# Kernel tuning notes

Hardware: AMD Instinct MI355X
Metric: run time of the kernel (lower is better)

## Reference

```python
import jax, jax.numpy as jnp
import numpy as np

STATE_DIM = 512
HIDDEN = 256
ACTION = 8
BATCH = 32768
LN_EPS = 1e-5


def setup_inputs() -> dict:
    key = jax.random.key(0)
    ks = jax.random.split(key, 24)
    s = 0.02
    inp = {
        'initial_state': jax.random.normal(ks[0], (BATCH, STATE_DIM), jnp.float32),
        'final_state': jax.random.normal(ks[1], (BATCH, STATE_DIM), jnp.float32),
        'horizon': 10,
        # fc: Linear(1024->256), LayerNorm(256), ReLU, Linear(256->256), ReLU
        'W1': jax.random.normal(ks[2], (HIDDEN, 2 * STATE_DIM), jnp.float32) * s,
        'b1': jnp.zeros((HIDDEN,), jnp.float32),
        'ln_g': jnp.ones((HIDDEN,), jnp.float32),
        'ln_b': jnp.zeros((HIDDEN,), jnp.float32),
        'W2': jax.random.normal(ks[3], (HIDDEN, HIDDEN), jnp.float32) * s,
        'b2': jnp.zeros((HIDDEN,), jnp.float32),
        # GRU layer 0 (input=ACTION) and layer 1 (input=HIDDEN)
        'Wih0': jax.random.normal(ks[4], (3 * HIDDEN, ACTION), jnp.float32) * s,
        'Whh0': jax.random.normal(ks[5], (3 * HIDDEN, HIDDEN), jnp.float32) * s,
        'bih0': jnp.zeros((3 * HIDDEN,), jnp.float32),
        'bhh0': jnp.zeros((3 * HIDDEN,), jnp.float32),
        'Wih1': jax.random.normal(ks[6], (3 * HIDDEN, HIDDEN), jnp.float32) * s,
        'Whh1': jax.random.normal(ks[7], (3 * HIDDEN, HIDDEN), jnp.float32) * s,
        'bih1': jnp.zeros((3 * HIDDEN,), jnp.float32),
        'bhh1': jnp.zeros((3 * HIDDEN,), jnp.float32),
        # fc_action: 256 -> 8
        'Wa': jax.random.normal(ks[8], (ACTION, HIDDEN), jnp.float32) * s,
        'ba': jnp.zeros((ACTION,), jnp.float32),
        # fc_init_hidden: 256 -> 512
        'Winit': jax.random.normal(ks[9], (2 * HIDDEN, HIDDEN), jnp.float32) * s,
        'binit': jnp.zeros((2 * HIDDEN,), jnp.float32),
    }
    return inp


def _gru_cell(x, h, Wih, Whh, bih, bhh):
    # torch.nn.GRU cell: gates ordered [r, z, n]
    gi = x @ Wih.T + bih              # [B, 3H]
    gh = h @ Whh.T + bhh              # [B, 3H]
    i_r, i_z, i_n = jnp.split(gi, 3, axis=-1)
    h_r, h_z, h_n = jnp.split(gh, 3, axis=-1)
    r = jax.nn.sigmoid(i_r + h_r)
    z = jax.nn.sigmoid(i_z + h_z)
    n = jnp.tanh(i_n + r * h_n)
    return (1.0 - z) * n + z * h


def reference(initial_state, final_state, horizon, W1, b1, ln_g, ln_b, W2, b2,
              Wih0, Whh0, bih0, bhh0, Wih1, Whh1, bih1, bhh1, Wa, ba, Winit, binit):
    B = initial_state.shape[0]
    combined = jnp.concatenate([initial_state, final_state], axis=-1)  # [B, 2*state]
    h = combined @ W1.T + b1
    mu = jnp.mean(h, axis=-1, keepdims=True)
    var = jnp.var(h, axis=-1, keepdims=True)
    h = (h - mu) * jax.lax.rsqrt(var + LN_EPS) * ln_g + ln_b
    h = jax.nn.relu(h)
    h = jax.nn.relu(h @ W2.T + b2)    # [B, H]

    # Replicates torch .view(2, B, H) on a [B, 2H] tensor (row-major reshape)
    hidden = jnp.reshape(h @ Winit.T + binit, (2, B, HIDDEN))
    h0, h1 = hidden[0], hidden[1]
    a0 = jnp.zeros((B, ACTION), initial_state.dtype)

    def step(carry, _):
        h0, h1, a = carry
        h0n = _gru_cell(a, h0, Wih0, Whh0, bih0, bhh0)
        h1n = _gru_cell(h0n, h1, Wih1, Whh1, bih1, bhh1)
        logits = h1n @ Wa.T + ba       # [B, A]
        a_next = jax.nn.softmax(logits, axis=-1)
        return (h0n, h1n, a_next), logits

    _, logits_seq = jax.lax.scan(step, (h0, h1, a0), None, length=horizon)
    return jnp.transpose(logits_seq, (1, 0, 2))  # [B, horizon, A]
```

## Files before the change

### kernel.cpp

```cpp
#include <hip/hip_runtime.h>


#define HS 264

typedef __attribute__((ext_vector_type(8))) short short8;
typedef __attribute__((ext_vector_type(4))) float fvec4;

__device__ __forceinline__ float bf2f(unsigned short u) {
    union { unsigned int u; float f; } x; x.u = ((unsigned int)u) << 16; return x.f;
}
__device__ __forceinline__ unsigned short f2bf(float f) {
    union { float f; unsigned int u; } x; x.f = f;
    unsigned int r = x.u + 0x7fffu + ((x.u >> 16) & 1u);
    return (unsigned short)(r >> 16);
}
__device__ __forceinline__ float sigm(float x)   { return __builtin_amdgcn_rcpf(1.f + __expf(-x)); }
__device__ __forceinline__ float tanh_f(float x) { return 2.f * __builtin_amdgcn_rcpf(1.f + __expf(-2.f * x)) - 1.f; }

__device__ __forceinline__ short8 ld8(const unsigned short* p) {
    return *reinterpret_cast<const short8*>(p);
}
__device__ __forceinline__ fvec4 mfma16(short8 a, short8 b, fvec4 c) {
    return __builtin_amdgcn_mfma_f32_16x16x32_bf16(a, b, c, 0, 0, 0);
}
__device__ __forceinline__ fvec4 splat4(float v) {
    fvec4 r = {v, v, v, v}; return r;
}

__device__ __forceinline__ int packoff(int e, int K) {
    const int n = e / K, k = e % K;
    return (((n >> 4) * (K >> 5) + (k >> 5)) << 9)
         + (((((k >> 3) & 3) << 4) | (n & 15)) << 3) + (k & 7);
}

__global__ __launch_bounds__(256) void k_prep(
    const float* __restrict__ W1, const float* __restrict__ W2,
    const float* __restrict__ Winit, const float* __restrict__ Wih0,
    const float* __restrict__ Whh0, const float* __restrict__ Wih1,
    const float* __restrict__ Whh1, const float* __restrict__ Wa,
    unsigned short* __restrict__ wb)
{
    int i = blockIdx.x * 256 + threadIdx.x;
    if (i >= 1056768) return;
    float v; int dst;
    if (i < 262144) {
        v = W1[i];                dst = packoff(i, 1024);
    } else if (i < 327680) {
        int e = i - 262144;  v = W2[e];    dst = 262144 + packoff(e, 256);
    } else if (i < 458752) {
        int e = i - 327680;  v = Winit[e]; dst = 327680 + packoff(e, 256);
    } else if (i < 464896) {
        v = Wih0[i - 458752];     dst = i;
    } else if (i < 661504) {
        int e = i - 464896;  v = Whh0[e];  dst = 464896 + packoff(e, 256);
    } else if (i < 858112) {
        int e = i - 661504;  v = Wih1[e];  dst = 661504 + packoff(e, 256);
    } else if (i < 1054720) {
        int e = i - 858112;  v = Whh1[e];  dst = 858112 + packoff(e, 256);
    } else {
        v = Wa[i - 1054720];      dst = i;
    }
    wb[dst] = f2bf(v);
}

__global__ __launch_bounds__(512, 2) void k_encode(
    const float* __restrict__ ini, const float* __restrict__ fin,
    const unsigned short* __restrict__ W1b, const float* __restrict__ b1,
    const float* __restrict__ lng, const float* __restrict__ lnb,
    const unsigned short* __restrict__ W2b, const float* __restrict__ b2,
    const unsigned short* __restrict__ Winitb, const float* __restrict__ binit,
    unsigned short* __restrict__ h0g, unsigned short* __restrict__ h1g)
{
    __shared__ unsigned short hb[64 * HS];
    __shared__ unsigned short at[2][64 * 40];
    __shared__ float ps[64][8][2];
    __shared__ float st[64][2];
    const int tid = threadIdx.x, lane = tid & 63, w = tid >> 6;
    const int l15 = lane & 15, q = lane >> 4;
    const int rows0 = blockIdx.x * 64;
    const int c0 = w * 32;
    const fvec4 fz = {0.f, 0.f, 0.f, 0.f};

    const int srow = tid >> 3, sseg = (tid & 7) * 4;

    fvec4 acc[4][2];
#pragma unroll
    for (int rt = 0; rt < 4; ++rt) { acc[rt][0] = fz; acc[rt][1] = fz; }
    {
        const float* src0 = ini + (rows0 + srow) * 512 + sseg;
        fvec4 v = *reinterpret_cast<const fvec4*>(src0);
        union { unsigned short s[4]; unsigned long long u; } p;
        p.s[0] = f2bf(v[0]); p.s[1] = f2bf(v[1]); p.s[2] = f2bf(v[2]); p.s[3] = f2bf(v[3]);
        *reinterpret_cast<unsigned long long*>(&at[0][srow * 40 + sseg]) = p.u;
    }
    __syncthreads();
#pragma unroll 1
    for (int kc = 0; kc < 32; ++kc) {
        const int buf = kc & 1;
        if (kc < 31) {
            const int k0 = (kc + 1) * 32 + sseg;
            const float* src = (k0 < 512) ? (ini + (rows0 + srow) * 512 + k0)
                                          : (fin + (rows0 + srow) * 512 + (k0 - 512));
            fvec4 v = *reinterpret_cast<const fvec4*>(src);
            union { unsigned short s[4]; unsigned long long u; } p;
            p.s[0] = f2bf(v[0]); p.s[1] = f2bf(v[1]); p.s[2] = f2bf(v[2]); p.s[3] = f2bf(v[3]);
            *reinterpret_cast<unsigned long long*>(&at[buf ^ 1][srow * 40 + sseg]) = p.u;
        }
        short8 b8a = ld8(W1b + (((w * 2 + 0) * 32 + kc) * 64 + lane) * 8);
        short8 b8b = ld8(W1b + (((w * 2 + 1) * 32 + kc) * 64 + lane) * 8);
        short8 a8[4];
#pragma unroll
        for (int rt = 0; rt < 4; ++rt)
            a8[rt] = ld8(&at[buf][(rt * 16 + l15) * 40 + q * 8]);
#pragma unroll
        for (int rt = 0; rt < 4; ++rt) {
            acc[rt][0] = mfma16(a8[rt], b8a, acc[rt][0]);
            acc[rt][1] = mfma16(a8[rt], b8b, acc[rt][1]);
        }
        __syncthreads();
    }
    float bv[2] = { b1[c0 + l15], b1[c0 + 16 + l15] };
#pragma unroll
    for (int rt = 0; rt < 4; ++rt)
#pragma unroll
        for (int r = 0; r < 4; ++r) {
            float s = 0.f, s2 = 0.f;
#pragma unroll
            for (int ct = 0; ct < 2; ++ct) {
                float v = acc[rt][ct][r] + bv[ct];
                acc[rt][ct][r] = v;
                s += v; s2 += v * v;
            }
#pragma unroll
            for (int off = 1; off < 16; off <<= 1) {
                s  += __shfl_xor(s,  off, 64);
                s2 += __shfl_xor(s2, off, 64);
            }
            if (l15 == 0) {
                int row = rt * 16 + q * 4 + r;
                ps[row][w][0] = s; ps[row][w][1] = s2;
            }
        }
    __syncthreads();
    if (tid < 64) {
        float s = 0.f, s2 = 0.f;
#pragma unroll
        for (int j = 0; j < 8; ++j) { s += ps[tid][j][0]; s2 += ps[tid][j][1]; }
        float mu = s * (1.f / 256.f);
        float var = s2 * (1.f / 256.f) - mu * mu;
        st[tid][0] = mu; st[tid][1] = rsqrtf(var + 1e-5f);
    }
    __syncthreads();
    {
        float gv[2]  = { lng[c0 + l15], lng[c0 + 16 + l15] };
        float bbv[2] = { lnb[c0 + l15], lnb[c0 + 16 + l15] };
#pragma unroll
        for (int rt = 0; rt < 4; ++rt)
#pragma unroll
            for (int ct = 0; ct < 2; ++ct)
#pragma unroll
                for (int r = 0; r < 4; ++r) {
                    int row = rt * 16 + q * 4 + r;
                    float v = (acc[rt][ct][r] - st[row][0]) * st[row][1] * gv[ct] + bbv[ct];
                    v = fmaxf(v, 0.f);
                    hb[row * HS + c0 + ct * 16 + l15] = f2bf(v);
                }
    }
    __syncthreads();
    fvec4 acc2[4][2];
#pragma unroll
    for (int rt = 0; rt < 4; ++rt) { acc2[rt][0] = fz; acc2[rt][1] = fz; }
#pragma unroll 2
    for (int kc = 0; kc < 8; ++kc) {
        const int k0 = kc * 32 + q * 8;
        short8 a8[4];
#pragma unroll
        for (int rt = 0; rt < 4; ++rt) a8[rt] = ld8(hb + (rt * 16 + l15) * HS + k0);
#pragma unroll
        for (int ct = 0; ct < 2; ++ct) {
            short8 b8 = ld8(W2b + (((w * 2 + ct) * 8 + kc) * 64 + lane) * 8);
#pragma unroll
            for (int rt = 0; rt < 4; ++rt) acc2[rt][ct] = mfma16(a8[rt], b8, acc2[rt][ct]);
        }
    }
    {
        float b2v[2] = { b2[c0 + l15], b2[c0 + 16 + l15] };
        unsigned short stg[4][2][4];
#pragma unroll
        for (int rt = 0; rt < 4; ++rt)
#pragma unroll
            for (int ct = 0; ct < 2; ++ct)
#pragma unroll
                for (int r = 0; r < 4; ++r)
                    stg[rt][ct][r] = f2bf(fmaxf(acc2[rt][ct][r] + b2v[ct], 0.f));
        __syncthreads();
#pragma unroll
        for (int rt = 0; rt < 4; ++rt)
#pragma unroll
            for (int ct = 0; ct < 2; ++ct)
#pragma unroll
                for (int r = 0; r < 4; ++r)
                    hb[(rt * 16 + q * 4 + r) * HS + c0 + ct * 16 + l15] = stg[rt][ct][r];
    }
    __syncthreads();
    fvec4 a3[4][4];
#pragma unroll
    for (int rt = 0; rt < 4; ++rt)
#pragma unroll
        for (int ct = 0; ct < 4; ++ct) a3[rt][ct] = fz;
#pragma unroll 1
    for (int kc = 0; kc < 8; ++kc) {
        const int k0 = kc * 32 + q * 8;
        short8 a8[4];
#pragma unroll
        for (int rt = 0; rt < 4; ++rt) a8[rt] = ld8(hb + (rt * 16 + l15) * HS + k0);
#pragma unroll
        for (int ct = 0; ct < 4; ++ct) {
            short8 b8 = ld8(Winitb + (((w * 4 + ct) * 8 + kc) * 64 + lane) * 8);
#pragma unroll
            for (int rt = 0; rt < 4; ++rt) a3[rt][ct] = mfma16(a8[rt], b8, a3[rt][ct]);
        }
    }
    const int c0i = w * 64;
#pragma unroll
    for (int ct = 0; ct < 4; ++ct) {
        const int j = c0i + ct * 16 + l15;
        const float bz = binit[j];
        const int half = j >> 8, cc = j & 255;
#pragma unroll
        for (int rt = 0; rt < 4; ++rt)
#pragma unroll
            for (int r = 0; r < 4; ++r) {
                const int i = rows0 + rt * 16 + q * 4 + r;
                const unsigned short v = f2bf(a3[rt][ct][r] + bz);
                if (i < 16384) h0g[(2 * i + half) * 256 + cc] = v;
                else           h1g[(2 * (i - 16384) + half) * 256 + cc] = v;
            }
    }
}

__global__ __launch_bounds__(512, 4) void k_roll(
    const unsigned short* __restrict__ h0g, const unsigned short* __restrict__ h1g,
    const unsigned short* __restrict__ Wih0b, const unsigned short* __restrict__ Whh0b,
    const unsigned short* __restrict__ Wih1b, const unsigned short* __restrict__ Whh1b,
    const unsigned short* __restrict__ Wab,
    const float* __restrict__ bih0, const float* __restrict__ bhh0,
    const float* __restrict__ bih1, const float* __restrict__ bhh1,
    const float* __restrict__ ba, float* __restrict__ out)
{
    __shared__ unsigned short h0s[64 * HS];
    __shared__ unsigned short h1s[64 * HS];
    __shared__ unsigned short avs[64 * 8];
    __shared__ float ldsb[2048];
    const int tid = threadIdx.x, lane = tid & 63, w = tid >> 6;
    const int l15 = lane & 15, q = lane >> 4;
    const int rows0 = blockIdx.x * 64;
    const int cb = w * 32;
    const fvec4 fz = {0.f, 0.f, 0.f, 0.f};
    const short8 z8 = {0,0,0,0,0,0,0,0};

    for (int it = tid; it < 64 * 32; it += 512) {
        const int row = it >> 5, g = (it & 31) * 8;
        *reinterpret_cast<short8*>(&h0s[row * HS + g]) = ld8(h0g + (rows0 + row) * 256 + g);
        *reinterpret_cast<short8*>(&h1s[row * HS + g]) = ld8(h1g + (rows0 + row) * 256 + g);
    }
    if (tid < 256) {
        const int j = tid;
        ldsb[j]       = bih0[j] + bhh0[j];
        ldsb[256 + j] = bih0[256 + j] + bhh0[256 + j];
        ldsb[512 + j] = bih0[512 + j];
        ldsb[768 + j] = bhh0[512 + j];
    } else {
        const int j = tid - 256;
        ldsb[1024 + j] = bih1[j] + bhh1[j];
        ldsb[1280 + j] = bih1[256 + j] + bhh1[256 + j];
        ldsb[1536 + j] = bih1[512 + j];
        ldsb[1792 + j] = bhh1[512 + j];
    }
    const float bav = ba[l15 & 7];
    __syncthreads();

    for (int t = 0; t < 10; ++t) {
        unsigned int st0[16];
#pragma unroll 1
        for (int p = 0; p < 2; ++p) {
            const int c = cb + p * 16 + l15;
            fvec4 aR[4], aZ[4], aNi[4], aNh[4];
            {
                const float vr = ldsb[c],       vz = ldsb[256 + c];
                const float vi = ldsb[512 + c], vh = ldsb[768 + c];
#pragma unroll
                for (int rt = 0; rt < 4; ++rt) {
                    aR[rt]  = splat4(vr);
                    aZ[rt]  = splat4(vz);
                    aNi[rt] = splat4(vi);
                    aNh[rt] = splat4(vh);
                }
            }
#pragma unroll 1
            for (int kc = 0; kc < 8; ++kc) {
                const int k0 = kc * 32 + q * 8;
                const unsigned short* wp =
                    Whh0b + ((((w * 2 + p) * 8 + kc) * 64 + lane) * 8);
                const short8 wr = ld8(wp);
                const short8 wz = ld8(wp + 65536);
                const short8 wn = ld8(wp + 131072);
#pragma unroll
                for (int rt = 0; rt < 4; ++rt) {
                    const short8 ah = ld8(h0s + (rt * 16 + l15) * HS + k0);
                    aR[rt]  = mfma16(ah, wr, aR[rt]);
                    aZ[rt]  = mfma16(ah, wz, aZ[rt]);
                    aNh[rt] = mfma16(ah, wn, aNh[rt]);
                }
            }
            if (t > 0) {
                const unsigned short* wp = Wih0b + c * 8;
                const short8 wr = ld8(wp);
                const short8 wz = ld8(wp + 2048);
                const short8 wn = ld8(wp + 4096);
#pragma unroll
                for (int rt = 0; rt < 4; ++rt) {
                    short8 v = ld8(avs + (rt * 16 + l15) * 8);
                    const short8 av = (q == 0) ? v : z8;
                    aR[rt]  = mfma16(av, wr, aR[rt]);
                    aZ[rt]  = mfma16(av, wz, aZ[rt]);
                    aNi[rt] = mfma16(av, wn, aNi[rt]);
                }
            }
#pragma unroll
            for (int rt = 0; rt < 4; ++rt)
#pragma unroll
                for (int r = 0; r < 4; ++r) {
                    const int row = rt * 16 + q * 4 + r;
                    const float hold = bf2f(h0s[row * HS + c]);
                    const float rr = sigm(aR[rt][r]);
                    const float zz = sigm(aZ[rt][r]);
                    const float nn = tanh_f(aNi[rt][r] + rr * aNh[rt][r]);
                    const unsigned int v = f2bf((1.f - zz) * nn + zz * hold);
                    st0[rt * 4 + r] = p ? (st0[rt * 4 + r] | (v << 16)) : v;
                }
        }
        __syncthreads();
#pragma unroll
        for (int rt = 0; rt < 4; ++rt)
#pragma unroll
            for (int r = 0; r < 4; ++r) {
                const int row = rt * 16 + q * 4 + r;
                const unsigned int v = st0[rt * 4 + r];
                h0s[row * HS + cb + l15]      = (unsigned short)v;
                h0s[row * HS + cb + 16 + l15] = (unsigned short)(v >> 16);
            }
        __syncthreads();
        unsigned int st1[16];
#pragma unroll 1
        for (int p = 0; p < 2; ++p) {
            const int c = cb + p * 16 + l15;
            fvec4 aR[4], aZ[4], aNi[4], aNh[4];
            {
                const float vr = ldsb[1024 + c], vz = ldsb[1280 + c];
                const float vi = ldsb[1536 + c], vh = ldsb[1792 + c];
#pragma unroll
                for (int rt = 0; rt < 4; ++rt) {
                    aR[rt]  = splat4(vr);
                    aZ[rt]  = splat4(vz);
                    aNi[rt] = splat4(vi);
                    aNh[rt] = splat4(vh);
                }
            }
#pragma unroll 1
            for (int kc = 0; kc < 8; ++kc) {
                const int k0 = kc * 32 + q * 8;
                const unsigned short* wi =
                    Wih1b + ((((w * 2 + p) * 8 + kc) * 64 + lane) * 8);
                const short8 wir = ld8(wi);
                const short8 wiz = ld8(wi + 65536);
                const short8 win = ld8(wi + 131072);
#pragma unroll
                for (int rt = 0; rt < 4; ++rt) {
                    const short8 ai = ld8(h0s + (rt * 16 + l15) * HS + k0);
                    aR[rt]  = mfma16(ai, wir, aR[rt]);
                    aZ[rt]  = mfma16(ai, wiz, aZ[rt]);
                    aNi[rt] = mfma16(ai, win, aNi[rt]);
                }
            }
#pragma unroll 1
            for (int kc = 0; kc < 8; ++kc) {
                const int k0 = kc * 32 + q * 8;
                const unsigned short* wh =
                    Whh1b + ((((w * 2 + p) * 8 + kc) * 64 + lane) * 8);
                const short8 whr = ld8(wh);
                const short8 whz = ld8(wh + 65536);
                const short8 whn = ld8(wh + 131072);
#pragma unroll
                for (int rt = 0; rt < 4; ++rt) {
                    const short8 ah = ld8(h1s + (rt * 16 + l15) * HS + k0);
                    aR[rt]  = mfma16(ah, whr, aR[rt]);
                    aZ[rt]  = mfma16(ah, whz, aZ[rt]);
                    aNh[rt] = mfma16(ah, whn, aNh[rt]);
                }
            }
#pragma unroll
            for (int rt = 0; rt < 4; ++rt)
#pragma unroll
                for (int r = 0; r < 4; ++r) {
                    const int row = rt * 16 + q * 4 + r;
                    const float hold = bf2f(h1s[row * HS + c]);
                    const float rr = sigm(aR[rt][r]);
                    const float zz = sigm(aZ[rt][r]);
                    const float nn = tanh_f(aNi[rt][r] + rr * aNh[rt][r]);
                    const unsigned int v = f2bf((1.f - zz) * nn + zz * hold);
                    st1[rt * 4 + r] = p ? (st1[rt * 4 + r] | (v << 16)) : v;
                }
        }
        __syncthreads();
#pragma unroll
        for (int rt = 0; rt < 4; ++rt)
#pragma unroll
            for (int r = 0; r < 4; ++r) {
                const int row = rt * 16 + q * 4 + r;
                const unsigned int v = st1[rt * 4 + r];
                h1s[row * HS + cb + l15]      = (unsigned short)v;
                h1s[row * HS + cb + 16 + l15] = (unsigned short)(v >> 16);
            }
        __syncthreads();
        if (w < 4) {
            fvec4 f = fz;
#pragma unroll 1
            for (int kc = 0; kc < 8; ++kc) {
                const int k0 = kc * 32 + q * 8;
                short8 a8 = ld8(h1s + (w * 16 + l15) * HS + k0);
                short8 b8 = ld8(Wab + (l15 & 7) * 256 + k0);
                f = mfma16(a8, b8, f);
            }
#pragma unroll
            for (int r = 0; r < 4; ++r) {
                float s = f[r] + bav;
                float m = s;
                m = fmaxf(m, __shfl_xor(m, 1, 64));
                m = fmaxf(m, __shfl_xor(m, 2, 64));
                m = fmaxf(m, __shfl_xor(m, 4, 64));
                float e = __expf(s - m);
                float se = e;
                se += __shfl_xor(se, 1, 64);
                se += __shfl_xor(se, 2, 64);
                se += __shfl_xor(se, 4, 64);
                if (l15 < 8) {
                    const int lrow = w * 16 + q * 4 + r;
                    out[(rows0 + lrow) * 80 + t * 8 + l15] = s;
                    avs[lrow * 8 + l15] = f2bf(e * __builtin_amdgcn_rcpf(se));
                }
            }
        }
        __syncthreads();
    }
}

extern "C" void kernel_launch(void* const* d_in, const int* in_sizes, int n_in,
                              void* d_out, int out_size, void* d_ws, size_t ws_size,
                              hipStream_t stream)
{
    const float* ini   = (const float*)d_in[0];
    const float* fin   = (const float*)d_in[1];
    const float* W1    = (const float*)d_in[3];
    const float* b1    = (const float*)d_in[4];
    const float* lng   = (const float*)d_in[5];
    const float* lnb   = (const float*)d_in[6];
    const float* W2    = (const float*)d_in[7];
    const float* b2    = (const float*)d_in[8];
    const float* Wih0  = (const float*)d_in[9];
    const float* Whh0  = (const float*)d_in[10];
    const float* bih0  = (const float*)d_in[11];
    const float* bhh0  = (const float*)d_in[12];
    const float* Wih1  = (const float*)d_in[13];
    const float* Whh1  = (const float*)d_in[14];
    const float* bih1  = (const float*)d_in[15];
    const float* bhh1  = (const float*)d_in[16];
    const float* Wa    = (const float*)d_in[17];
    const float* ba    = (const float*)d_in[18];
    const float* Winit = (const float*)d_in[19];
    const float* binit = (const float*)d_in[20];
    float* out = (float*)d_out;

    char* ws = (char*)d_ws;
    unsigned short* wb     = (unsigned short*)ws;
    unsigned short* W1b    = wb;
    unsigned short* W2b    = wb + 262144;
    unsigned short* Winitb = wb + 327680;
    unsigned short* Wih0b  = wb + 458752;
    unsigned short* Whh0b  = wb + 464896;
    unsigned short* Wih1b  = wb + 661504;
    unsigned short* Whh1b  = wb + 858112;
    unsigned short* Wab    = wb + 1054720;
    unsigned short* h0g = (unsigned short*)(ws + 2113536);
    unsigned short* h1g = (unsigned short*)(ws + 18890752);

    k_prep<<<dim3(4128), dim3(256), 0, stream>>>(W1, W2, Winit, Wih0, Whh0, Wih1, Whh1, Wa, wb);
    k_encode<<<dim3(512), dim3(512), 0, stream>>>(ini, fin, W1b, b1, lng, lnb, W2b, b2,
                                                  Winitb, binit, h0g, h1g);
    k_roll<<<dim3(512), dim3(512), 0, stream>>>(h0g, h1g, Wih0b, Whh0b, Wih1b, Whh1b, Wab,
                                                bih0, bhh0, bih1, bhh1, ba, out);
}
```

Measured before the change: 763.3 us.

## Double-buffer GRU hidden state in LDS with XOR swizzle, drop extra barriers

The recurrent kernel now keeps two copies of the h0 and h1 tiles in shared memory and ping-pongs between them each timestep. Each thread writes its new hidden values straight into the next buffer, which removes the register staging and two of the four barriers per step. Row padding is replaced by an XOR swizzle to avoid bank conflicts, and the K loops are unrolled by 4. In exchange, shared memory use roughly doubles and the launch bound is lowered to 2 blocks per SM, which may cut occupancy.

```diff
diff --git a/kernel.cpp b/kernel.cpp
--- a/kernel.cpp
+++ b/kernel.cpp
@@ -2,6 +2,7 @@
 
 
 #define HS 264
+#define HR 256
 
 typedef __attribute__((ext_vector_type(8))) short short8;
 typedef __attribute__((ext_vector_type(4))) float fvec4;
@@ -25,6 +26,9 @@
 }
 __device__ __forceinline__ fvec4 splat4(float v) {
     fvec4 r = {v, v, v, v}; return r;
+}
+__device__ __forceinline__ int swz(int row, int k) {
+    return row * HR + (k ^ ((row & 7) << 3));
 }
 
 __device__ __forceinline__ int packoff(int e, int K) {
@@ -239,7 +243,7 @@
     }
 }
 
-__global__ __launch_bounds__(512, 4) void k_roll(
+__global__ __launch_bounds__(512, 2) void k_roll(
     const unsigned short* __restrict__ h0g, const unsigned short* __restrict__ h1g,
     const unsigned short* __restrict__ Wih0b, const unsigned short* __restrict__ Whh0b,
     const unsigned short* __restrict__ Wih1b, const unsigned short* __restrict__ Whh1b,
@@ -248,8 +252,8 @@
     const float* __restrict__ bih1, const float* __restrict__ bhh1,
     const float* __restrict__ ba, float* __restrict__ out)
 {
-    __shared__ unsigned short h0s[64 * HS];
-    __shared__ unsigned short h1s[64 * HS];
+    __shared__ unsigned short h0sb[2][64 * HR];
+    __shared__ unsigned short h1sb[2][64 * HR];
     __shared__ unsigned short avs[64 * 8];
     __shared__ float ldsb[2048];
     const int tid = threadIdx.x, lane = tid & 63, w = tid >> 6;
@@ -261,8 +265,9 @@
 
     for (int it = tid; it < 64 * 32; it += 512) {
         const int row = it >> 5, g = (it & 31) * 8;
-        *reinterpret_cast<short8*>(&h0s[row * HS + g]) = ld8(h0g + (rows0 + row) * 256 + g);
-        *reinterpret_cast<short8*>(&h1s[row * HS + g]) = ld8(h1g + (rows0 + row) * 256 + g);
+        const int d = swz(row, g);
+        *reinterpret_cast<short8*>(&h0sb[0][d]) = ld8(h0g + (rows0 + row) * 256 + g);
+        *reinterpret_cast<short8*>(&h1sb[0][d]) = ld8(h1g + (rows0 + row) * 256 + g);
     }
     if (tid < 256) {
         const int j = tid;
@@ -281,7 +286,11 @@
     __syncthreads();
 
     for (int t = 0; t < 10; ++t) {
-        unsigned int st0[16];
+        const int cur = t & 1, nxt = cur ^ 1;
+        const unsigned short* h0c = h0sb[cur];
+        unsigned short*       h0n = h0sb[nxt];
+        const unsigned short* h1c = h1sb[cur];
+        unsigned short*       h1n = h1sb[nxt];
 #pragma unroll 1
         for (int p = 0; p < 2; ++p) {
             const int c = cb + p * 16 + l15;
@@ -297,7 +306,21 @@
                     aNh[rt] = splat4(vh);
                 }
             }
-#pragma unroll 1
+            if (t > 0) {
+                const unsigned short* wp = Wih0b + c * 8;
+                const short8 wr = ld8(wp);
+                const short8 wz = ld8(wp + 2048);
+                const short8 wn = ld8(wp + 4096);
+#pragma unroll
+                for (int rt = 0; rt < 4; ++rt) {
+                    short8 v = ld8(avs + (rt * 16 + l15) * 8);
+                    const short8 av = (q == 0) ? v : z8;
+                    aR[rt]  = mfma16(av, wr, aR[rt]);
+                    aZ[rt]  = mfma16(av, wz, aZ[rt]);
+                    aNi[rt] = mfma16(av, wn, aNi[rt]);
+                }
+            }
+#pragma unroll 4
             for (int kc = 0; kc < 8; ++kc) {
                 const int k0 = kc * 32 + q * 8;
                 const unsigned short* wp =
@@ -307,51 +330,25 @@
                 const short8 wn = ld8(wp + 131072);
 #pragma unroll
                 for (int rt = 0; rt < 4; ++rt) {
-                    const short8 ah = ld8(h0s + (rt * 16 + l15) * HS + k0);
+                    const short8 ah = ld8(h0c + swz(rt * 16 + l15, k0));
                     aR[rt]  = mfma16(ah, wr, aR[rt]);
                     aZ[rt]  = mfma16(ah, wz, aZ[rt]);
                     aNh[rt] = mfma16(ah, wn, aNh[rt]);
                 }
             }
-            if (t > 0) {
-                const unsigned short* wp = Wih0b + c * 8;
-                const short8 wr = ld8(wp);
-                const short8 wz = ld8(wp + 2048);
-                const short8 wn = ld8(wp + 4096);
-#pragma unroll
-                for (int rt = 0; rt < 4; ++rt) {
-                    short8 v = ld8(avs + (rt * 16 + l15) * 8);
-                    const short8 av = (q == 0) ? v : z8;
-                    aR[rt]  = mfma16(av, wr, aR[rt]);
-                    aZ[rt]  = mfma16(av, wz, aZ[rt]);
-                    aNi[rt] = mfma16(av, wn, aNi[rt]);
-                }
-            }
 #pragma unroll
             for (int rt = 0; rt < 4; ++rt)
 #pragma unroll
                 for (int r = 0; r < 4; ++r) {
                     const int row = rt * 16 + q * 4 + r;
-                    const float hold = bf2f(h0s[row * HS + c]);
+                    const float hold = bf2f(h0c[swz(row, c)]);
                     const float rr = sigm(aR[rt][r]);
                     const float zz = sigm(aZ[rt][r]);
                     const float nn = tanh_f(aNi[rt][r] + rr * aNh[rt][r]);
-                    const unsigned int v = f2bf((1.f - zz) * nn + zz * hold);
-                    st0[rt * 4 + r] = p ? (st0[rt * 4 + r] | (v << 16)) : v;
+                    h0n[swz(row, c)] = f2bf((1.f - zz) * nn + zz * hold);
                 }
         }
         __syncthreads();
-#pragma unroll
-        for (int rt = 0; rt < 4; ++rt)
-#pragma unroll
-            for (int r = 0; r < 4; ++r) {
-                const int row = rt * 16 + q * 4 + r;
-                const unsigned int v = st0[rt * 4 + r];
-                h0s[row * HS + cb + l15]      = (unsigned short)v;
-                h0s[row * HS + cb + 16 + l15] = (unsigned short)(v >> 16);
-            }
-        __syncthreads();
-        unsigned int st1[16];
 #pragma unroll 1
         for (int p = 0; p < 2; ++p) {
             const int c = cb + p * 16 + l15;
@@ -367,7 +364,7 @@
                     aNh[rt] = splat4(vh);
                 }
             }
-#pragma unroll 1
+#pragma unroll 4
             for (int kc = 0; kc < 8; ++kc) {
                 const int k0 = kc * 32 + q * 8;
                 const unsigned short* wi =
@@ -377,13 +374,13 @@
                 const short8 win = ld8(wi + 131072);
 #pragma unroll
                 for (int rt = 0; rt < 4; ++rt) {
-                    const short8 ai = ld8(h0s + (rt * 16 + l15) * HS + k0);
+                    const short8 ai = ld8(h0n + swz(rt * 16 + l15, k0));
                     aR[rt]  = mfma16(ai, wir, aR[rt]);
                     aZ[rt]  = mfma16(ai, wiz, aZ[rt]);
                     aNi[rt] = mfma16(ai, win, aNi[rt]);
                 }
             }
-#pragma unroll 1
+#pragma unroll 4
             for (int kc = 0; kc < 8; ++kc) {
                 const int k0 = kc * 32 + q * 8;
                 const unsigned short* wh =
@@ -393,7 +390,7 @@
                 const short8 whn = ld8(wh + 131072);
 #pragma unroll
                 for (int rt = 0; rt < 4; ++rt) {
-                    const short8 ah = ld8(h1s + (rt * 16 + l15) * HS + k0);
+                    const short8 ah = ld8(h1c + swz(rt * 16 + l15, k0));
                     aR[rt]  = mfma16(ah, whr, aR[rt]);
                     aZ[rt]  = mfma16(ah, whz, aZ[rt]);
                     aNh[rt] = mfma16(ah, whn, aNh[rt]);
@@ -404,31 +401,20 @@
 #pragma unroll
                 for (int r = 0; r < 4; ++r) {
                     const int row = rt * 16 + q * 4 + r;
-                    const float hold = bf2f(h1s[row * HS + c]);
+                    const float hold = bf2f(h1c[swz(row, c)]);
                     const float rr = sigm(aR[rt][r]);
                     const float zz = sigm(aZ[rt][r]);
                     const float nn = tanh_f(aNi[rt][r] + rr * aNh[rt][r]);
-                    const unsigned int v = f2bf((1.f - zz) * nn + zz * hold);
-                    st1[rt * 4 + r] = p ? (st1[rt * 4 + r] | (v << 16)) : v;
-                }
-        }
-        __syncthreads();
-#pragma unroll
-        for (int rt = 0; rt < 4; ++rt)
-#pragma unroll
-            for (int r = 0; r < 4; ++r) {
-                const int row = rt * 16 + q * 4 + r;
-                const unsigned int v = st1[rt * 4 + r];
-                h1s[row * HS + cb + l15]      = (unsigned short)v;
-                h1s[row * HS + cb + 16 + l15] = (unsigned short)(v >> 16);
-            }
+                    h1n[swz(row, c)] = f2bf((1.f - zz) * nn + zz * hold);
+                }
+        }
         __syncthreads();
         if (w < 4) {
             fvec4 f = fz;
 #pragma unroll 1
             for (int kc = 0; kc < 8; ++kc) {
                 const int k0 = kc * 32 + q * 8;
-                short8 a8 = ld8(h1s + (w * 16 + l15) * HS + k0);
+                short8 a8 = ld8(h1n + swz(w * 16 + l15, k0));
                 short8 b8 = ld8(Wab + (l15 & 7) * 256 + k0);
                 f = mfma16(a8, b8, f);
             }
```

After: 724.1 us. -5.1%, faster.
